# Performance work log

Hardware: AMD Instinct MI355X
Metric: run time of the kernel (lower is better)

The kernel has to match this reference:

```python
import jax, jax.numpy as jnp
import numpy as np

N_ITER = 3


def squash(v):
    # v: [..., out_C]; scale by ||v||^2/(1+||v||^2) and normalize by ||v||
    sq = jnp.sum(v * v, axis=-1, keepdims=True)
    return (sq / (1.0 + sq)) * v / jnp.sqrt(sq)


def setup_inputs() -> dict:
    key = jax.random.key(0)
    k1, k2 = jax.random.split(key)
    B, n_nodes, n_caps, in_C, out_C = 64, 2048, 32, 16, 32
    x = jax.random.normal(k1, (B, n_nodes, in_C), dtype=jnp.float32)
    route_weights = 0.1 * jax.random.normal(k2, (n_nodes, n_caps, in_C, out_C), dtype=jnp.float32)
    return {"x": x, "route_weights": route_weights}


def reference(x, route_weights):
    # priors: [B, n_nodes, n_caps, out_C]
    priors = jnp.einsum('bni,nkio->bnko', x, route_weights)
    logits = jnp.zeros_like(priors)
    outputs = None
    for i in range(N_ITER):
        probs = jax.nn.softmax(logits, axis=2)            # over n_caps
        s = jnp.sum(probs * priors, axis=1, keepdims=True)  # [B,1,n_caps,out_C]
        outputs = squash(s)
        if i != N_ITER - 1:
            delta = jnp.sum(priors * outputs, axis=-1, keepdims=True)
            logits = logits + delta
    return outputs
```

## Files before the change

kernel.cpp:

```cpp
#include <hip/hip_runtime.h>
#include <math.h>


#define BATCH 64
#define NN    2048
#define NK    32
#define NI    16
#define NO    32

#define PNB   16
#define NSETS (NN / PNB)

typedef __bf16 bf16x8 __attribute__((ext_vector_type(8)));
typedef float  f32x16 __attribute__((ext_vector_type(16)));

__device__ __forceinline__ unsigned short f2bf(float f) {
    unsigned int x = __float_as_uint(f);
    unsigned int lsb = (x >> 16) & 1u;
    x += 0x7fffu + lsb;
    return (unsigned short)(x >> 16);
}
__device__ __forceinline__ float bflo(unsigned int u) { return __uint_as_float(u << 16); }
__device__ __forceinline__ float bfhi(unsigned int u) { return __uint_as_float(u & 0xffff0000u); }


__global__ __launch_bounds__(1024) void zero_kernel(float* __restrict__ p) {
    p[blockIdx.x * 1024 + threadIdx.x] = 0.f;
}

__global__ __launch_bounds__(256) void xt_kernel(const float* __restrict__ xg,
                                                 unsigned short* __restrict__ xT) {
    int id = blockIdx.x * 256 + threadIdx.x;
    int b = id >> 13;
    int rem = id & 8191;
    int n = rem >> 2;
    int i4 = rem & 3;
    float4 v = *(const float4*)(xg + ((size_t)b * NN + n) * NI + i4 * 4);
    ushort4 o;
    o.x = f2bf(v.x); o.y = f2bf(v.y); o.z = f2bf(v.z); o.w = f2bf(v.w);
    *(ushort4*)(xT + ((size_t)n * BATCH + b) * NI + i4 * 4) = o;
}

__global__ __launch_bounds__(256) void wqt_kernel(const float* __restrict__ Wg,
                                                  unsigned short* __restrict__ wq) {
    const int w    = threadIdx.x >> 6;
    const int lane = threadIdx.x & 63;
    const int task = blockIdx.x * 4 + w;
    const int o  = lane & 31;
    const int ih = lane >> 5;
    const float* src = Wg + (size_t)task * (NI * NO);
    unsigned short d[8];
#pragma unroll
    for (int j = 0; j < 8; ++j)
        d[j] = f2bf(src[(ih * 8 + j) * NO + o]);
    *(uint4*)(wq + (size_t)task * (NO * NI) + o * NI + ih * 8) = *(uint4*)d;
}

template <int PASS>
__global__ __launch_bounds__(1024) void fused_pass(
    const unsigned short* __restrict__ xT,
    const unsigned short* __restrict__ wq,
    const float* __restrict__ outv,
    float* __restrict__ logits0,
    float* __restrict__ s_glob)
{
    __shared__ float delta_lds[2][32 * 33];

    const int tid  = threadIdx.x;
    const int w    = tid >> 6;
    const int lane = tid & 63;
    const int l5   = lane & 31;
    const int h5   = lane >> 5;
    const int set  = blockIdx.x;
    const int hb   = blockIdx.y;
    const int k0   = 2 * w, k1 = 2 * w + 1;
    const int gb5  = hb * 32 + l5;
    const int sb   = tid >> 5;
    const int sk   = tid & 31;
    const int nbase = set * PNB;

    unsigned orp0[8], orp1[8];
    if constexpr (PASS >= 1) {
#pragma unroll
        for (int q = 0; q < 8; ++q) {
            const int oA = ((2*q) & 3) + 8 * ((2*q) >> 2) + 4 * h5;
            const int oB = ((2*q+1) & 3) + 8 * ((2*q+1) >> 2) + 4 * h5;
            float a0 = outv[(k0 * NO + oA) * BATCH + gb5];
            float b0 = outv[(k0 * NO + oB) * BATCH + gb5];
            float a1 = outv[(k1 * NO + oA) * BATCH + gb5];
            float b1 = outv[(k1 * NO + oB) * BATCH + gb5];
            orp0[q] = (unsigned)f2bf(a0) | ((unsigned)f2bf(b0) << 16);
            orp1[q] = (unsigned)f2bf(a1) | ((unsigned)f2bf(b1) << 16);
        }
    }

    float sa0[16], sa1[16];
#pragma unroll
    for (int r = 0; r < 16; ++r) { sa0[r] = 0.f; sa1[r] = 0.f; }

    bf16x8 aN, b0N, b1N;
    float gN = 0.f;
    {
        const int n = nbase;
        b0N = *(const bf16x8*)(wq + (size_t)n * (NK * NO * NI) + k0 * (NO * NI) + l5 * NI + h5 * 8);
        b1N = *(const bf16x8*)(wq + (size_t)n * (NK * NO * NI) + k1 * (NO * NI) + l5 * NI + h5 * 8);
        aN  = *(const bf16x8*)(xT + (size_t)n * (BATCH * NI) + gb5 * NI + h5 * 8);
        if constexpr (PASS == 2)
            gN = logits0[(size_t)n * (BATCH * NK) + hb * 1024 + tid];
    }

    int buf = 0;
    for (int j = 0; j < PNB; ++j) {
        const int n = nbase + j;
        const bf16x8 aC = aN, b0C = b0N, b1C = b1N;
        const float gC = gN;
        if (j < PNB - 1) {
            const int n2 = n + 1;
            b0N = *(const bf16x8*)(wq + (size_t)n2 * (NK * NO * NI) + k0 * (NO * NI) + l5 * NI + h5 * 8);
            b1N = *(const bf16x8*)(wq + (size_t)n2 * (NK * NO * NI) + k1 * (NO * NI) + l5 * NI + h5 * 8);
            aN  = *(const bf16x8*)(xT + (size_t)n2 * (BATCH * NI) + gb5 * NI + h5 * 8);
            if constexpr (PASS == 2)
                gN = logits0[(size_t)n2 * (BATCH * NK) + hb * 1024 + tid];
        }

        f32x16 c0, c1;
#pragma unroll
        for (int r = 0; r < 16; ++r) { c0[r] = 0.f; c1[r] = 0.f; }
        c0 = __builtin_amdgcn_mfma_f32_32x32x16_bf16(b0C, aC, c0, 0, 0, 0);
        c1 = __builtin_amdgcn_mfma_f32_32x32x16_bf16(b1C, aC, c1, 0, 0, 0);

        if constexpr (PASS == 0) {
#pragma unroll
            for (int r = 0; r < 16; ++r) { sa0[r] += c0[r]; sa1[r] += c1[r]; }
        } else {
            float d0 = 0.f, d1 = 0.f;
#pragma unroll
            for (int r = 0; r < 16; ++r) {
                const unsigned u0 = orp0[r >> 1], u1 = orp1[r >> 1];
                const float o0 = (r & 1) ? bfhi(u0) : bflo(u0);
                const float o1 = (r & 1) ? bfhi(u1) : bflo(u1);
                d0 = fmaf(c0[r], o0, d0);
                d1 = fmaf(c1[r], o1, d1);
            }
            d0 += __shfl_xor(d0, 32);
            d1 += __shfl_xor(d1, 32);

            delta_lds[buf][l5 * 33 + (h5 ? k1 : k0)] = h5 ? d1 : d0;
            __syncthreads();

            float l = delta_lds[buf][sb * 33 + sk];
            if constexpr (PASS == 1)
                logits0[(size_t)n * (BATCH * NK) + hb * 1024 + tid] = l;
            else
                l += gC;
            float e = __expf(l);
            float s = e;
#pragma unroll
            for (int mask = 1; mask < 32; mask <<= 1)
                s += __shfl_xor(s, mask);
            delta_lds[buf][sb * 33 + sk] = e / s;
            __syncthreads();

            const float p0 = delta_lds[buf][l5 * 33 + k0];
            const float p1 = delta_lds[buf][l5 * 33 + k1];
#pragma unroll
            for (int r = 0; r < 16; ++r) {
                sa0[r] = fmaf(p0, c0[r], sa0[r]);
                sa1[r] = fmaf(p1, c1[r], sa1[r]);
            }
            buf ^= 1;
        }
    }

    const float scale = (PASS == 0) ? (1.f / NK) : 1.f;
#pragma unroll
    for (int r = 0; r < 16; ++r) {
        const int o = (r & 3) + 8 * (r >> 2) + 4 * h5;
        atomicAdd(&s_glob[(k0 * NO + o) * BATCH + gb5], sa0[r] * scale);
        atomicAdd(&s_glob[(k1 * NO + o) * BATCH + gb5], sa1[r] * scale);
    }
}

template <int FINAL>
__global__ __launch_bounds__(1024) void reduce_squash2(
    float* __restrict__ s_glob,
    float* __restrict__ outv,
    float* __restrict__ outp)
{
    __shared__ float red[2048];
    __shared__ float coef[64];
    const int k = blockIdx.x;
    const int t = threadIdx.x;
    const int o = t >> 6;
    const int b = t & 63;
    float* base = s_glob + k * 2048;
    float va = base[o * 64 + b];
    float vb = base[(o + 16) * 64 + b];
    base[o * 64 + b] = 0.f;
    base[(o + 16) * 64 + b] = 0.f;
    red[o * 64 + b] = va * va;
    red[(o + 16) * 64 + b] = vb * vb;
    __syncthreads();
    if (t < 64) {
        float sq = 0.f;
#pragma unroll
        for (int oo = 0; oo < 32; ++oo) sq += red[oo * 64 + t];
        coef[t] = sq / ((1.f + sq) * sqrtf(sq));
    }
    __syncthreads();
    const float cf = coef[b];
    if (FINAL) {
        outp[b * 1024 + k * 32 + o]      = va * cf;
        outp[b * 1024 + k * 32 + o + 16] = vb * cf;
    } else {
        outv[k * 2048 + o * 64 + b]        = va * cf;
        outv[k * 2048 + (o + 16) * 64 + b] = vb * cf;
    }
}


#define LBB 32
#define LNCHUNK 8
#define LNBLK (NN / LNCHUNK)
#define LTHREADS 512
#define WK_STRIDE 516

template <int PASS>
__global__ __launch_bounds__(LTHREADS, 1) void legacy_pass(
    const float* __restrict__ xg, const float* __restrict__ Wg,
    const float* __restrict__ outvL, float* __restrict__ logits,
    float* __restrict__ partial)
{
    __shared__ float w_lds[NK * WK_STRIDE];
    __shared__ float x_lds[LBB][NI + 1];
    __shared__ float delta_lds[LBB][NK + 1];
    const int t = threadIdx.x, nb = blockIdx.x, bg = blockIdx.y;
    const int b0 = bg * LBB;
    const int k = t >> 4, bq = t & 15, bl0 = bq * 2, bl1 = bq * 2 + 1;
    float acc0[NO], acc1[NO];
#pragma unroll
    for (int o = 0; o < NO; ++o) { acc0[o] = 0.f; acc1[o] = 0.f; }
    float outr0[NO], outr1[NO];
    if constexpr (PASS >= 1) {
        const float4* o0 = (const float4*)&outvL[((b0 + bl0) * NK + k) * NO];
        const float4* o1 = (const float4*)&outvL[((b0 + bl1) * NK + k) * NO];
#pragma unroll
        for (int q = 0; q < NO / 4; ++q) {
            float4 a = o0[q]; float4 b = o1[q];
            outr0[4*q+0]=a.x; outr0[4*q+1]=a.y; outr0[4*q+2]=a.z; outr0[4*q+3]=a.w;
            outr1[4*q+0]=b.x; outr1[4*q+1]=b.y; outr1[4*q+2]=b.z; outr1[4*q+3]=b.w;
        }
    }
    for (int j = 0; j < LNCHUNK; ++j) {
        const int n = nb * LNCHUNK + j;
        __syncthreads();
        {
            const float4* src = (const float4*)(Wg + (size_t)n * (NK * NI * NO));
#pragma unroll
            for (int r = 0; r < (NK * NI * NO / 4) / LTHREADS; ++r) {
                int idx4 = t + r * LTHREADS;
                float4 v = src[idx4];
                int e = idx4 * 4, kk = e >> 9, rem = e & 511;
                *(float4*)&w_lds[kk * WK_STRIDE + rem] = v;
            }
        }
        { int bl = t >> 4, i = t & 15;
          x_lds[bl][i] = xg[((size_t)(b0 + bl) * NN + n) * NI + i]; }
        __syncthreads();
        if constexpr (PASS == 0) {
#pragma unroll
            for (int i = 0; i < NI; ++i) {
                float xa = x_lds[bl0][i], xb = x_lds[bl1][i];
                const float* wrow = &w_lds[k * WK_STRIDE + i * NO];
#pragma unroll
                for (int o = 0; o < NO; ++o) {
                    float w = wrow[o];
                    acc0[o] = fmaf(xa, w, acc0[o]);
                    acc1[o] = fmaf(xb, w, acc1[o]);
                }
            }
        } else {
            float pr0[NO], pr1[NO];
#pragma unroll
            for (int o = 0; o < NO; ++o) { pr0[o] = 0.f; pr1[o] = 0.f; }
#pragma unroll
            for (int i = 0; i < NI; ++i) {
                float xa = x_lds[bl0][i], xb = x_lds[bl1][i];
                const float* wrow = &w_lds[k * WK_STRIDE + i * NO];
#pragma unroll
                for (int o = 0; o < NO; ++o) {
                    float w = wrow[o];
                    pr0[o] = fmaf(xa, w, pr0[o]);
                    pr1[o] = fmaf(xb, w, pr1[o]);
                }
            }
            float d0 = 0.f, d1 = 0.f;
#pragma unroll
            for (int o = 0; o < NO; ++o) {
                d0 = fmaf(pr0[o], outr0[o], d0);
                d1 = fmaf(pr1[o], outr1[o], d1);
            }
            float l0 = d0, l1 = d1;
            const size_t li0 = ((size_t)(b0 + bl0) * NN + n) * NK + k;
            const size_t li1 = ((size_t)(b0 + bl1) * NN + n) * NK + k;
            if constexpr (PASS == 2) { l0 += logits[li0]; l1 += logits[li1]; }
            else { logits[li0] = d0; logits[li1] = d1; }
            delta_lds[bl0][k] = l0; delta_lds[bl1][k] = l1;
            __syncthreads();
            float m0 = -1e30f, m1 = -1e30f;
#pragma unroll
            for (int kk = 0; kk < NK; ++kk) {
                m0 = fmaxf(m0, delta_lds[bl0][kk]);
                m1 = fmaxf(m1, delta_lds[bl1][kk]);
            }
            float s0 = 0.f, s1 = 0.f;
#pragma unroll
            for (int kk = 0; kk < NK; ++kk) {
                s0 += __expf(delta_lds[bl0][kk] - m0);
                s1 += __expf(delta_lds[bl1][kk] - m1);
            }
            float p0 = __expf(l0 - m0) / s0;
            float p1 = __expf(l1 - m1) / s1;
#pragma unroll
            for (int o = 0; o < NO; ++o) {
                acc0[o] = fmaf(p0, pr0[o], acc0[o]);
                acc1[o] = fmaf(p1, pr1[o], acc1[o]);
            }
        }
    }
    const float scale = (PASS == 0) ? (1.f / NK) : 1.f;
    float4* p0 = (float4*)&partial[(((size_t)nb * BATCH + (b0 + bl0)) * NK + k) * NO];
    float4* p1 = (float4*)&partial[(((size_t)nb * BATCH + (b0 + bl1)) * NK + k) * NO];
#pragma unroll
    for (int q = 0; q < NO / 4; ++q) {
        float4 v0, v1;
        v0.x = acc0[4*q+0]*scale; v0.y = acc0[4*q+1]*scale;
        v0.z = acc0[4*q+2]*scale; v0.w = acc0[4*q+3]*scale;
        v1.x = acc1[4*q+0]*scale; v1.y = acc1[4*q+1]*scale;
        v1.z = acc1[4*q+2]*scale; v1.w = acc1[4*q+3]*scale;
        p0[q] = v0; p1[q] = v1;
    }
}

__global__ __launch_bounds__(256) void legacy_reduce(
    const float* __restrict__ partial, float* __restrict__ outf)
{
    const int tid = blockIdx.x * 256 + threadIdx.x;
    float v = 0.f;
    for (int nb = 0; nb < LNBLK; ++nb)
        v += partial[(size_t)nb * (BATCH * NK * NO) + tid];
    float sq = v * v;
#pragma unroll
    for (int off = 1; off < 32; off <<= 1) sq += __shfl_xor(sq, off);
    float coef = sq / ((1.f + sq) * sqrtf(sq));
    outf[tid] = v * coef;
}


extern "C" void kernel_launch(void* const* d_in, const int* in_sizes, int n_in,
                              void* d_out, int out_size, void* d_ws, size_t ws_size,
                              hipStream_t stream)
{
    const float* xg = (const float*)d_in[0];
    const float* Wg = (const float*)d_in[1];
    float* outp = (float*)d_out;
    char* ws = (char*)d_ws;

    const size_t SZ_WQ     = (size_t)NN * NK * NO * NI * 2;
    const size_t SZ_XT     = (size_t)NN * BATCH * NI * 2;
    const size_t SZ_LOGITS = (size_t)NN * BATCH * NK * 4;
    const size_t SZ_SG     = (size_t)NK * NO * BATCH * 4;
    const size_t SZ_OUTV   = (size_t)NK * NO * BATCH * 4;
    const size_t NEED = SZ_WQ + SZ_XT + SZ_LOGITS + SZ_SG + SZ_OUTV;

    if (ws_size >= NEED) {
        unsigned short* wq = (unsigned short*)ws;
        unsigned short* xT = (unsigned short*)(ws + SZ_WQ);
        float* logits0 = (float*)(ws + SZ_WQ + SZ_XT);
        float* s_glob  = (float*)(ws + SZ_WQ + SZ_XT + SZ_LOGITS);
        float* outv    = (float*)(ws + SZ_WQ + SZ_XT + SZ_LOGITS + SZ_SG);

        zero_kernel<<<64, 1024, 0, stream>>>(s_glob);
        xt_kernel<<<2048, 256, 0, stream>>>(xg, xT);
        wqt_kernel<<<16384, 256, 0, stream>>>(Wg, wq);

        dim3 pg(NSETS, 2);
        fused_pass<0><<<pg, 1024, 0, stream>>>(xT, wq, nullptr, nullptr, s_glob);
        reduce_squash2<0><<<32, 1024, 0, stream>>>(s_glob, outv, nullptr);
        fused_pass<1><<<pg, 1024, 0, stream>>>(xT, wq, outv, logits0, s_glob);
        reduce_squash2<0><<<32, 1024, 0, stream>>>(s_glob, outv, nullptr);
        fused_pass<2><<<pg, 1024, 0, stream>>>(xT, wq, outv, logits0, s_glob);
        reduce_squash2<1><<<32, 1024, 0, stream>>>(s_glob, nullptr, outp);
    } else {
        float* partial = (float*)ws;
        float* logits = (float*)(ws + (size_t)LNBLK * BATCH * NK * NO * 4);
        float* outvL = (float*)(ws + (size_t)LNBLK * BATCH * NK * NO * 4 + (size_t)BATCH * NN * NK * 4);
        dim3 grid(LNBLK, BATCH / LBB);
        const int rblocks = BATCH * NK * NO / 256;
        legacy_pass<0><<<grid, LTHREADS, 0, stream>>>(xg, Wg, nullptr, logits, partial);
        legacy_reduce<<<rblocks, 256, 0, stream>>>(partial, outvL);
        legacy_pass<1><<<grid, LTHREADS, 0, stream>>>(xg, Wg, outvL, logits, partial);
        legacy_reduce<<<rblocks, 256, 0, stream>>>(partial, outvL);
        legacy_pass<2><<<grid, LTHREADS, 0, stream>>>(xg, Wg, outvL, logits, partial);
        legacy_reduce<<<rblocks, 256, 0, stream>>>(partial, outp);
    }
}
```

Measured before the change: 380.0 us.

## Fuse routing passes into one persistent kernel with grid barriers and LDS-resident logits

```diff
diff --git a/kernel.cpp b/kernel.cpp
--- a/kernel.cpp
+++ b/kernel.cpp
@@ -10,9 +10,13 @@
 
 #define PNB   16
 #define NSETS (NN / PNB)
+#define NBLK  (NSETS * 2)
+#define XT_JS 528
 
 typedef __bf16 bf16x8 __attribute__((ext_vector_type(8)));
 typedef float  f32x16 __attribute__((ext_vector_type(16)));
+
+template <int N> struct IC { static constexpr int v = N; };
 
 __device__ __forceinline__ unsigned short f2bf(float f) {
     unsigned int x = __float_as_uint(f);
@@ -23,26 +27,22 @@
 __device__ __forceinline__ float bflo(unsigned int u) { return __uint_as_float(u << 16); }
 __device__ __forceinline__ float bfhi(unsigned int u) { return __uint_as_float(u & 0xffff0000u); }
 
-
-__global__ __launch_bounds__(1024) void zero_kernel(float* __restrict__ p) {
-    p[blockIdx.x * 1024 + threadIdx.x] = 0.f;
-}
-
-__global__ __launch_bounds__(256) void xt_kernel(const float* __restrict__ xg,
-                                                 unsigned short* __restrict__ xT) {
-    int id = blockIdx.x * 256 + threadIdx.x;
-    int b = id >> 13;
-    int rem = id & 8191;
-    int n = rem >> 2;
-    int i4 = rem & 3;
-    float4 v = *(const float4*)(xg + ((size_t)b * NN + n) * NI + i4 * 4);
-    ushort4 o;
-    o.x = f2bf(v.x); o.y = f2bf(v.y); o.z = f2bf(v.z); o.w = f2bf(v.w);
-    *(ushort4*)(xT + ((size_t)n * BATCH + b) * NI + i4 * 4) = o;
-}
-
-__global__ __launch_bounds__(256) void wqt_kernel(const float* __restrict__ Wg,
-                                                  unsigned short* __restrict__ wq) {
+__device__ __forceinline__ void grid_bar(unsigned* __restrict__ bar, int idx) {
+    __syncthreads();
+    if (threadIdx.x == 0) {
+        __builtin_amdgcn_fence(__ATOMIC_RELEASE, "agent");
+        __hip_atomic_fetch_add(&bar[idx], 1u, __ATOMIC_RELAXED, __HIP_MEMORY_SCOPE_AGENT);
+        while (__hip_atomic_load(&bar[idx], __ATOMIC_RELAXED, __HIP_MEMORY_SCOPE_AGENT) < NBLK)
+            __builtin_amdgcn_s_sleep(2);
+        __builtin_amdgcn_fence(__ATOMIC_ACQUIRE, "agent");
+    }
+    __syncthreads();
+}
+
+__global__ __launch_bounds__(256) void prep_kernel(const float* __restrict__ Wg,
+                                                   unsigned short* __restrict__ wq,
+                                                   float* __restrict__ sg3,
+                                                   unsigned* __restrict__ bar) {
     const int w    = threadIdx.x >> 6;
     const int lane = threadIdx.x & 63;
     const int task = blockIdx.x * 4 + w;
@@ -54,16 +54,24 @@
     for (int j = 0; j < 8; ++j)
         d[j] = f2bf(src[(ih * 8 + j) * NO + o]);
     *(uint4*)(wq + (size_t)task * (NO * NI) + o * NI + ih * 8) = *(uint4*)d;
-}
-
-template <int PASS>
-__global__ __launch_bounds__(1024) void fused_pass(
-    const unsigned short* __restrict__ xT,
+
+    if (blockIdx.x < 192) {
+        float4 z = {0.f, 0.f, 0.f, 0.f};
+        *(float4*)(sg3 + (size_t)blockIdx.x * 1024 + threadIdx.x * 4) = z;
+    }
+    if (blockIdx.x == 200 && threadIdx.x < 8) bar[threadIdx.x] = 0u;
+}
+
+
+__global__ __launch_bounds__(1024) void routing_mega(
+    const float* __restrict__ xg,
     const unsigned short* __restrict__ wq,
-    const float* __restrict__ outv,
-    float* __restrict__ logits0,
-    float* __restrict__ s_glob)
+    float* __restrict__ s_glob,
+    unsigned* __restrict__ bar,
+    float* __restrict__ outp)
 {
+    __shared__ unsigned short xt_lds[PNB * XT_JS];
+    __shared__ float logits_lds[PNB * 1024];
     __shared__ float delta_lds[2][32 * 33];
 
     const int tid  = threadIdx.x;
@@ -75,146 +83,162 @@
     const int hb   = blockIdx.y;
     const int k0   = 2 * w, k1 = 2 * w + 1;
     const int gb5  = hb * 32 + l5;
-    const int sb   = tid >> 5;
-    const int sk   = tid & 31;
+    const int sbt  = tid >> 5;
+    const int skt  = tid & 31;
     const int nbase = set * PNB;
 
+#pragma unroll
+    for (int rr = 0; rr < 2; ++rr) {
+        const int id  = tid + rr * 1024;
+        const int bl  = id >> 6;
+        const int rem = id & 63;
+        const int j   = rem >> 2;
+        const int i4  = rem & 3;
+        float4 v = *(const float4*)(xg + ((size_t)(hb * 32 + bl) * NN + (nbase + j)) * NI + i4 * 4);
+        ushort4 o4;
+        o4.x = f2bf(v.x); o4.y = f2bf(v.y); o4.z = f2bf(v.z); o4.w = f2bf(v.w);
+        *(ushort4*)(xt_lds + j * XT_JS + bl * 16 + i4 * 4) = o4;
+    }
+    __syncthreads();
+
     unsigned orp0[8], orp1[8];
-    if constexpr (PASS >= 1) {
+
+    auto build_orp = [&](const float* __restrict__ sbuf) {
+        float v0[16], v1[16];
+        float sq0 = 0.f, sq1 = 0.f;
+#pragma unroll
+        for (int r = 0; r < 16; ++r) {
+            const int o = (r & 3) + 8 * (r >> 2) + 4 * h5;
+            v0[r] = sbuf[(k0 * NO + o) * BATCH + gb5];
+            v1[r] = sbuf[(k1 * NO + o) * BATCH + gb5];
+            sq0 = fmaf(v0[r], v0[r], sq0);
+            sq1 = fmaf(v1[r], v1[r], sq1);
+        }
+        sq0 += __shfl_xor(sq0, 32);
+        sq1 += __shfl_xor(sq1, 32);
+        const float cf0 = sq0 / ((1.f + sq0) * sqrtf(sq0));
+        const float cf1 = sq1 / ((1.f + sq1) * sqrtf(sq1));
 #pragma unroll
         for (int q = 0; q < 8; ++q) {
-            const int oA = ((2*q) & 3) + 8 * ((2*q) >> 2) + 4 * h5;
-            const int oB = ((2*q+1) & 3) + 8 * ((2*q+1) >> 2) + 4 * h5;
-            float a0 = outv[(k0 * NO + oA) * BATCH + gb5];
-            float b0 = outv[(k0 * NO + oB) * BATCH + gb5];
-            float a1 = outv[(k1 * NO + oA) * BATCH + gb5];
-            float b1 = outv[(k1 * NO + oB) * BATCH + gb5];
-            orp0[q] = (unsigned)f2bf(a0) | ((unsigned)f2bf(b0) << 16);
-            orp1[q] = (unsigned)f2bf(a1) | ((unsigned)f2bf(b1) << 16);
-        }
-    }
-
-    float sa0[16], sa1[16];
-#pragma unroll
-    for (int r = 0; r < 16; ++r) { sa0[r] = 0.f; sa1[r] = 0.f; }
-
-    bf16x8 aN, b0N, b1N;
-    float gN = 0.f;
-    {
-        const int n = nbase;
-        b0N = *(const bf16x8*)(wq + (size_t)n * (NK * NO * NI) + k0 * (NO * NI) + l5 * NI + h5 * 8);
-        b1N = *(const bf16x8*)(wq + (size_t)n * (NK * NO * NI) + k1 * (NO * NI) + l5 * NI + h5 * 8);
-        aN  = *(const bf16x8*)(xT + (size_t)n * (BATCH * NI) + gb5 * NI + h5 * 8);
-        if constexpr (PASS == 2)
-            gN = logits0[(size_t)n * (BATCH * NK) + hb * 1024 + tid];
-    }
-
-    int buf = 0;
-    for (int j = 0; j < PNB; ++j) {
-        const int n = nbase + j;
-        const bf16x8 aC = aN, b0C = b0N, b1C = b1N;
-        const float gC = gN;
-        if (j < PNB - 1) {
-            const int n2 = n + 1;
-            b0N = *(const bf16x8*)(wq + (size_t)n2 * (NK * NO * NI) + k0 * (NO * NI) + l5 * NI + h5 * 8);
-            b1N = *(const bf16x8*)(wq + (size_t)n2 * (NK * NO * NI) + k1 * (NO * NI) + l5 * NI + h5 * 8);
-            aN  = *(const bf16x8*)(xT + (size_t)n2 * (BATCH * NI) + gb5 * NI + h5 * 8);
-            if constexpr (PASS == 2)
-                gN = logits0[(size_t)n2 * (BATCH * NK) + hb * 1024 + tid];
-        }
-
-        f32x16 c0, c1;
-#pragma unroll
-        for (int r = 0; r < 16; ++r) { c0[r] = 0.f; c1[r] = 0.f; }
-        c0 = __builtin_amdgcn_mfma_f32_32x32x16_bf16(b0C, aC, c0, 0, 0, 0);
-        c1 = __builtin_amdgcn_mfma_f32_32x32x16_bf16(b1C, aC, c1, 0, 0, 0);
-
-        if constexpr (PASS == 0) {
-#pragma unroll
-            for (int r = 0; r < 16; ++r) { sa0[r] += c0[r]; sa1[r] += c1[r]; }
-        } else {
-            float d0 = 0.f, d1 = 0.f;
-#pragma unroll
-            for (int r = 0; r < 16; ++r) {
-                const unsigned u0 = orp0[r >> 1], u1 = orp1[r >> 1];
-                const float o0 = (r & 1) ? bfhi(u0) : bflo(u0);
-                const float o1 = (r & 1) ? bfhi(u1) : bflo(u1);
-                d0 = fmaf(c0[r], o0, d0);
-                d1 = fmaf(c1[r], o1, d1);
-            }
-            d0 += __shfl_xor(d0, 32);
-            d1 += __shfl_xor(d1, 32);
-
-            delta_lds[buf][l5 * 33 + (h5 ? k1 : k0)] = h5 ? d1 : d0;
-            __syncthreads();
-
-            float l = delta_lds[buf][sb * 33 + sk];
-            if constexpr (PASS == 1)
-                logits0[(size_t)n * (BATCH * NK) + hb * 1024 + tid] = l;
-            else
-                l += gC;
-            float e = __expf(l);
-            float s = e;
-#pragma unroll
-            for (int mask = 1; mask < 32; mask <<= 1)
-                s += __shfl_xor(s, mask);
-            delta_lds[buf][sb * 33 + sk] = e / s;
-            __syncthreads();
-
-            const float p0 = delta_lds[buf][l5 * 33 + k0];
-            const float p1 = delta_lds[buf][l5 * 33 + k1];
-#pragma unroll
-            for (int r = 0; r < 16; ++r) {
-                sa0[r] = fmaf(p0, c0[r], sa0[r]);
-                sa1[r] = fmaf(p1, c1[r], sa1[r]);
-            }
-            buf ^= 1;
-        }
-    }
-
-    const float scale = (PASS == 0) ? (1.f / NK) : 1.f;
-#pragma unroll
-    for (int r = 0; r < 16; ++r) {
-        const int o = (r & 3) + 8 * (r >> 2) + 4 * h5;
-        atomicAdd(&s_glob[(k0 * NO + o) * BATCH + gb5], sa0[r] * scale);
-        atomicAdd(&s_glob[(k1 * NO + o) * BATCH + gb5], sa1[r] * scale);
-    }
-}
-
-template <int FINAL>
-__global__ __launch_bounds__(1024) void reduce_squash2(
-    float* __restrict__ s_glob,
-    float* __restrict__ outv,
-    float* __restrict__ outp)
-{
-    __shared__ float red[2048];
-    __shared__ float coef[64];
-    const int k = blockIdx.x;
-    const int t = threadIdx.x;
-    const int o = t >> 6;
-    const int b = t & 63;
-    float* base = s_glob + k * 2048;
-    float va = base[o * 64 + b];
-    float vb = base[(o + 16) * 64 + b];
-    base[o * 64 + b] = 0.f;
-    base[(o + 16) * 64 + b] = 0.f;
-    red[o * 64 + b] = va * va;
-    red[(o + 16) * 64 + b] = vb * vb;
-    __syncthreads();
-    if (t < 64) {
-        float sq = 0.f;
-#pragma unroll
-        for (int oo = 0; oo < 32; ++oo) sq += red[oo * 64 + t];
-        coef[t] = sq / ((1.f + sq) * sqrtf(sq));
-    }
-    __syncthreads();
-    const float cf = coef[b];
-    if (FINAL) {
+            orp0[q] = (unsigned)f2bf(v0[2 * q] * cf0) | ((unsigned)f2bf(v0[2 * q + 1] * cf0) << 16);
+            orp1[q] = (unsigned)f2bf(v1[2 * q] * cf1) | ((unsigned)f2bf(v1[2 * q + 1] * cf1) << 16);
+        }
+    };
+
+    auto run = [&](auto pcv) {
+        constexpr int PASS = decltype(pcv)::v;
+        float* __restrict__ sg = s_glob + PASS * (NK * NO * BATCH);
+
+        float sa0[16], sa1[16];
+#pragma unroll
+        for (int r = 0; r < 16; ++r) { sa0[r] = 0.f; sa1[r] = 0.f; }
+
+        bf16x8 b0N, b1N;
+        {
+            const int n = nbase;
+            b0N = *(const bf16x8*)(wq + (size_t)n * (NK * NO * NI) + k0 * (NO * NI) + l5 * NI + h5 * 8);
+            b1N = *(const bf16x8*)(wq + (size_t)n * (NK * NO * NI) + k1 * (NO * NI) + l5 * NI + h5 * 8);
+        }
+
+        int buf = 0;
+        for (int j = 0; j < PNB; ++j) {
+            const bf16x8 b0C = b0N, b1C = b1N;
+            if (j < PNB - 1) {
+                const int n2 = nbase + j + 1;
+                b0N = *(const bf16x8*)(wq + (size_t)n2 * (NK * NO * NI) + k0 * (NO * NI) + l5 * NI + h5 * 8);
+                b1N = *(const bf16x8*)(wq + (size_t)n2 * (NK * NO * NI) + k1 * (NO * NI) + l5 * NI + h5 * 8);
+            }
+            const bf16x8 aC = *(const bf16x8*)(xt_lds + j * XT_JS + l5 * 16 + h5 * 8);
+
+            f32x16 c0, c1;
+#pragma unroll
+            for (int r = 0; r < 16; ++r) { c0[r] = 0.f; c1[r] = 0.f; }
+            c0 = __builtin_amdgcn_mfma_f32_32x32x16_bf16(b0C, aC, c0, 0, 0, 0);
+            c1 = __builtin_amdgcn_mfma_f32_32x32x16_bf16(b1C, aC, c1, 0, 0, 0);
+
+            if constexpr (PASS == 0) {
+#pragma unroll
+                for (int r = 0; r < 16; ++r) { sa0[r] += c0[r]; sa1[r] += c1[r]; }
+            } else {
+                float d0 = 0.f, d1 = 0.f;
+#pragma unroll
+                for (int r = 0; r < 16; ++r) {
+                    const unsigned u0 = orp0[r >> 1], u1 = orp1[r >> 1];
+                    const float o0 = (r & 1) ? bfhi(u0) : bflo(u0);
+                    const float o1 = (r & 1) ? bfhi(u1) : bflo(u1);
+                    d0 = fmaf(c0[r], o0, d0);
+                    d1 = fmaf(c1[r], o1, d1);
+                }
+                d0 += __shfl_xor(d0, 32);
+                d1 += __shfl_xor(d1, 32);
+
+                delta_lds[buf][l5 * 33 + (h5 ? k1 : k0)] = h5 ? d1 : d0;
+                __syncthreads();
+
+                float l = delta_lds[buf][sbt * 33 + skt];
+                if constexpr (PASS == 1)
+                    logits_lds[j * 1024 + sbt * 32 + skt] = l;
+                else
+                    l += logits_lds[j * 1024 + sbt * 32 + skt];
+                float e = __expf(l);
+                float s = e;
+#pragma unroll
+                for (int mask = 1; mask < 32; mask <<= 1)
+                    s += __shfl_xor(s, mask);
+                delta_lds[buf][sbt * 33 + skt] = e / s;
+                __syncthreads();
+
+                const float p0 = delta_lds[buf][l5 * 33 + k0];
+                const float p1 = delta_lds[buf][l5 * 33 + k1];
+#pragma unroll
+                for (int r = 0; r < 16; ++r) {
+                    sa0[r] = fmaf(p0, c0[r], sa0[r]);
+                    sa1[r] = fmaf(p1, c1[r], sa1[r]);
+                }
+                buf ^= 1;
+            }
+        }
+
+        const float scale = (PASS == 0) ? (1.f / NK) : 1.f;
+#pragma unroll
+        for (int r = 0; r < 16; ++r) {
+            const int o = (r & 3) + 8 * (r >> 2) + 4 * h5;
+            atomicAdd(&sg[(k0 * NO + o) * BATCH + gb5], sa0[r] * scale);
+            atomicAdd(&sg[(k1 * NO + o) * BATCH + gb5], sa1[r] * scale);
+        }
+    };
+
+    run(IC<0>{});
+    grid_bar(bar, 0);
+    build_orp(s_glob);
+    run(IC<1>{});
+    grid_bar(bar, 1);
+    build_orp(s_glob + NK * NO * BATCH);
+    run(IC<2>{});
+    grid_bar(bar, 2);
+
+    if (hb == 0 && set < NK) {
+        const int k = set;
+        float* red = &delta_lds[0][0];
+        float* cfp = red + 2048;
+        const float* base = s_glob + 2 * (NK * NO * BATCH) + k * (NO * BATCH);
+        const int o = tid >> 6;
+        const int b = tid & 63;
+        const float va = base[o * 64 + b];
+        const float vb = base[(o + 16) * 64 + b];
+        red[o * 64 + b] = va * va;
+        red[(o + 16) * 64 + b] = vb * vb;
+        __syncthreads();
+        if (tid < 64) {
+            float sq = 0.f;
+#pragma unroll
+            for (int oo = 0; oo < 32; ++oo) sq += red[oo * 64 + tid];
+            cfp[tid] = sq / ((1.f + sq) * sqrtf(sq));
+        }
+        __syncthreads();
+        const float cf = cfp[b];
         outp[b * 1024 + k * 32 + o]      = va * cf;
         outp[b * 1024 + k * 32 + o + 16] = vb * cf;
-    } else {
-        outv[k * 2048 + o * 64 + b]        = va * cf;
-        outv[k * 2048 + (o + 16) * 64 + b] = vb * cf;
     }
 }
 
@@ -366,31 +390,18 @@
     float* outp = (float*)d_out;
     char* ws = (char*)d_ws;
 
-    const size_t SZ_WQ     = (size_t)NN * NK * NO * NI * 2;
-    const size_t SZ_XT     = (size_t)NN * BATCH * NI * 2;
-    const size_t SZ_LOGITS = (size_t)NN * BATCH * NK * 4;
-    const size_t SZ_SG     = (size_t)NK * NO * BATCH * 4;
-    const size_t SZ_OUTV   = (size_t)NK * NO * BATCH * 4;
-    const size_t NEED = SZ_WQ + SZ_XT + SZ_LOGITS + SZ_SG + SZ_OUTV;
+    const size_t SZ_WQ  = (size_t)NN * NK * NO * NI * 2;
+    const size_t SZ_SG3 = 3 * (size_t)NK * NO * BATCH * 4;
+    const size_t SZ_BAR = 256;
+    const size_t NEED = SZ_WQ + SZ_SG3 + SZ_BAR;
 
     if (ws_size >= NEED) {
         unsigned short* wq = (unsigned short*)ws;
-        unsigned short* xT = (unsigned short*)(ws + SZ_WQ);
-        float* logits0 = (float*)(ws + SZ_WQ + SZ_XT);
-        float* s_glob  = (float*)(ws + SZ_WQ + SZ_XT + SZ_LOGITS);
-        float* outv    = (float*)(ws + SZ_WQ + SZ_XT + SZ_LOGITS + SZ_SG);
-
-        zero_kernel<<<64, 1024, 0, stream>>>(s_glob);
-        xt_kernel<<<2048, 256, 0, stream>>>(xg, xT);
-        wqt_kernel<<<16384, 256, 0, stream>>>(Wg, wq);
-
-        dim3 pg(NSETS, 2);
-        fused_pass<0><<<pg, 1024, 0, stream>>>(xT, wq, nullptr, nullptr, s_glob);
-        reduce_squash2<0><<<32, 1024, 0, stream>>>(s_glob, outv, nullptr);
-        fused_pass<1><<<pg, 1024, 0, stream>>>(xT, wq, outv, logits0, s_glob);
-        reduce_squash2<0><<<32, 1024, 0, stream>>>(s_glob, outv, nullptr);
-        fused_pass<2><<<pg, 1024, 0, stream>>>(xT, wq, outv, logits0, s_glob);
-        reduce_squash2<1><<<32, 1024, 0, stream>>>(s_glob, nullptr, outp);
+        float* sg3 = (float*)(ws + SZ_WQ);
+        unsigned* bar = (unsigned*)(ws + SZ_WQ + SZ_SG3);
+
+        prep_kernel<<<16384, 256, 0, stream>>>(Wg, wq, sg3, bar);
+        routing_mega<<<dim3(NSETS, 2), 1024, 0, stream>>>(xg, wq, sg3, bar, outp);
     } else {
         float* partial = (float*)ws;
         float* logits = (float*)(ws + (size_t)LNBLK * BATCH * NK * NO * 4);
```

After: 477.8 us. 1.26x slower.

## Fuse x transpose into fused passes and replace atomics with partial-sum reduction

Applied to the files above, without the earlier changes.

```diff
diff --git a/kernel.cpp b/kernel.cpp
--- a/kernel.cpp
+++ b/kernel.cpp
@@ -10,6 +10,7 @@
 
 #define PNB   16
 #define NSETS (NN / PNB)
+#define XT_JS 528
 
 typedef __bf16 bf16x8 __attribute__((ext_vector_type(8)));
 typedef float  f32x16 __attribute__((ext_vector_type(16)));
@@ -22,24 +23,6 @@
 }
 __device__ __forceinline__ float bflo(unsigned int u) { return __uint_as_float(u << 16); }
 __device__ __forceinline__ float bfhi(unsigned int u) { return __uint_as_float(u & 0xffff0000u); }
-
-
-__global__ __launch_bounds__(1024) void zero_kernel(float* __restrict__ p) {
-    p[blockIdx.x * 1024 + threadIdx.x] = 0.f;
-}
-
-__global__ __launch_bounds__(256) void xt_kernel(const float* __restrict__ xg,
-                                                 unsigned short* __restrict__ xT) {
-    int id = blockIdx.x * 256 + threadIdx.x;
-    int b = id >> 13;
-    int rem = id & 8191;
-    int n = rem >> 2;
-    int i4 = rem & 3;
-    float4 v = *(const float4*)(xg + ((size_t)b * NN + n) * NI + i4 * 4);
-    ushort4 o;
-    o.x = f2bf(v.x); o.y = f2bf(v.y); o.z = f2bf(v.z); o.w = f2bf(v.w);
-    *(ushort4*)(xT + ((size_t)n * BATCH + b) * NI + i4 * 4) = o;
-}
 
 __global__ __launch_bounds__(256) void wqt_kernel(const float* __restrict__ Wg,
                                                   unsigned short* __restrict__ wq) {
@@ -58,12 +41,13 @@
 
 template <int PASS>
 __global__ __launch_bounds__(1024) void fused_pass(
-    const unsigned short* __restrict__ xT,
+    const float* __restrict__ xg,
     const unsigned short* __restrict__ wq,
     const float* __restrict__ outv,
     float* __restrict__ logits0,
-    float* __restrict__ s_glob)
+    float* __restrict__ part)
 {
+    __shared__ unsigned short xt_lds[PNB * XT_JS];
     __shared__ float delta_lds[2][32 * 33];
 
     const int tid  = threadIdx.x;
@@ -79,6 +63,20 @@
     const int sk   = tid & 31;
     const int nbase = set * PNB;
 
+#pragma unroll
+    for (int rr = 0; rr < 2; ++rr) {
+        const int id  = tid + rr * 1024;
+        const int bl  = id >> 6;
+        const int rem = id & 63;
+        const int j   = rem >> 2;
+        const int i4  = rem & 3;
+        float4 v = *(const float4*)(xg + ((size_t)(hb * 32 + bl) * NN + (nbase + j)) * NI + i4 * 4);
+        ushort4 o4;
+        o4.x = f2bf(v.x); o4.y = f2bf(v.y); o4.z = f2bf(v.z); o4.w = f2bf(v.w);
+        *(ushort4*)(xt_lds + j * XT_JS + bl * 16 + i4 * 4) = o4;
+    }
+    __syncthreads();
+
     unsigned orp0[8], orp1[8];
     if constexpr (PASS >= 1) {
 #pragma unroll
@@ -98,13 +96,12 @@
 #pragma unroll
     for (int r = 0; r < 16; ++r) { sa0[r] = 0.f; sa1[r] = 0.f; }
 
-    bf16x8 aN, b0N, b1N;
+    bf16x8 b0N, b1N;
     float gN = 0.f;
     {
         const int n = nbase;
         b0N = *(const bf16x8*)(wq + (size_t)n * (NK * NO * NI) + k0 * (NO * NI) + l5 * NI + h5 * 8);
         b1N = *(const bf16x8*)(wq + (size_t)n * (NK * NO * NI) + k1 * (NO * NI) + l5 * NI + h5 * 8);
-        aN  = *(const bf16x8*)(xT + (size_t)n * (BATCH * NI) + gb5 * NI + h5 * 8);
         if constexpr (PASS == 2)
             gN = logits0[(size_t)n * (BATCH * NK) + hb * 1024 + tid];
     }
@@ -112,16 +109,16 @@
     int buf = 0;
     for (int j = 0; j < PNB; ++j) {
         const int n = nbase + j;
-        const bf16x8 aC = aN, b0C = b0N, b1C = b1N;
+        const bf16x8 b0C = b0N, b1C = b1N;
         const float gC = gN;
         if (j < PNB - 1) {
             const int n2 = n + 1;
             b0N = *(const bf16x8*)(wq + (size_t)n2 * (NK * NO * NI) + k0 * (NO * NI) + l5 * NI + h5 * 8);
             b1N = *(const bf16x8*)(wq + (size_t)n2 * (NK * NO * NI) + k1 * (NO * NI) + l5 * NI + h5 * 8);
-            aN  = *(const bf16x8*)(xT + (size_t)n2 * (BATCH * NI) + gb5 * NI + h5 * 8);
             if constexpr (PASS == 2)
                 gN = logits0[(size_t)n2 * (BATCH * NK) + hb * 1024 + tid];
         }
+        const bf16x8 aC = *(const bf16x8*)(xt_lds + j * XT_JS + l5 * 16 + h5 * 8);
 
         f32x16 c0, c1;
 #pragma unroll
@@ -173,48 +170,53 @@
     }
 
     const float scale = (PASS == 0) ? (1.f / NK) : 1.f;
+    float* pb = part + ((size_t)(hb * NSETS + set) << 15);
 #pragma unroll
     for (int r = 0; r < 16; ++r) {
         const int o = (r & 3) + 8 * (r >> 2) + 4 * h5;
-        atomicAdd(&s_glob[(k0 * NO + o) * BATCH + gb5], sa0[r] * scale);
-        atomicAdd(&s_glob[(k1 * NO + o) * BATCH + gb5], sa1[r] * scale);
+        pb[(k0 * NO + o) * 32 + l5] = sa0[r] * scale;
+        pb[(k1 * NO + o) * 32 + l5] = sa1[r] * scale;
     }
 }
 
 template <int FINAL>
-__global__ __launch_bounds__(1024) void reduce_squash2(
-    float* __restrict__ s_glob,
+__global__ __launch_bounds__(1024) void reduce_squash3(
+    const float* __restrict__ part,
     float* __restrict__ outv,
     float* __restrict__ outp)
 {
-    __shared__ float red[2048];
-    __shared__ float coef[64];
-    const int k = blockIdx.x;
-    const int t = threadIdx.x;
-    const int o = t >> 6;
-    const int b = t & 63;
-    float* base = s_glob + k * 2048;
-    float va = base[o * 64 + b];
-    float vb = base[(o + 16) * 64 + b];
-    base[o * 64 + b] = 0.f;
-    base[(o + 16) * 64 + b] = 0.f;
-    red[o * 64 + b] = va * va;
-    red[(o + 16) * 64 + b] = vb * vb;
+    __shared__ float s_lds[32 * 33];
+    __shared__ float cf_lds[32];
+    const int k  = blockIdx.x;
+    const int hb = blockIdx.y;
+    const int t  = threadIdx.x;
+    const int o  = t >> 5;
+    const int b  = t & 31;
+
+    const float* src = part + ((size_t)hb * NSETS << 15) + (k << 10) + (o << 5) + b;
+    float v0 = 0.f, v1 = 0.f, v2 = 0.f, v3 = 0.f;
+#pragma unroll 4
+    for (int s = 0; s < NSETS; s += 4) {
+        v0 += src[(size_t)(s + 0) << 15];
+        v1 += src[(size_t)(s + 1) << 15];
+        v2 += src[(size_t)(s + 2) << 15];
+        v3 += src[(size_t)(s + 3) << 15];
+    }
+    const float v = (v0 + v1) + (v2 + v3);
+    s_lds[o * 33 + b] = v;
     __syncthreads();
-    if (t < 64) {
+    if (t < 32) {
         float sq = 0.f;
 #pragma unroll
-        for (int oo = 0; oo < 32; ++oo) sq += red[oo * 64 + t];
-        coef[t] = sq / ((1.f + sq) * sqrtf(sq));
+        for (int oo = 0; oo < 32; ++oo) { const float x = s_lds[oo * 33 + t]; sq = fmaf(x, x, sq); }
+        cf_lds[t] = sq / ((1.f + sq) * sqrtf(sq));
     }
     __syncthreads();
-    const float cf = coef[b];
     if (FINAL) {
-        outp[b * 1024 + k * 32 + o]      = va * cf;
-        outp[b * 1024 + k * 32 + o + 16] = vb * cf;
+        const int bq = t >> 5, oq = t & 31;
+        outp[(size_t)(hb * 32 + bq) * 1024 + k * 32 + oq] = s_lds[oq * 33 + bq] * cf_lds[bq];
     } else {
-        outv[k * 2048 + o * 64 + b]        = va * cf;
-        outv[k * 2048 + (o + 16) * 64 + b] = vb * cf;
+        outv[k * 2048 + o * 64 + hb * 32 + b] = v * cf_lds[b];
     }
 }
 
@@ -367,30 +369,27 @@
     char* ws = (char*)d_ws;
 
     const size_t SZ_WQ     = (size_t)NN * NK * NO * NI * 2;
-    const size_t SZ_XT     = (size_t)NN * BATCH * NI * 2;
+    const size_t SZ_PART   = (size_t)256 * 32768 * 4;
     const size_t SZ_LOGITS = (size_t)NN * BATCH * NK * 4;
-    const size_t SZ_SG     = (size_t)NK * NO * BATCH * 4;
     const size_t SZ_OUTV   = (size_t)NK * NO * BATCH * 4;
-    const size_t NEED = SZ_WQ + SZ_XT + SZ_LOGITS + SZ_SG + SZ_OUTV;
+    const size_t NEED = SZ_WQ + SZ_PART + SZ_LOGITS + SZ_OUTV;
 
     if (ws_size >= NEED) {
         unsigned short* wq = (unsigned short*)ws;
-        unsigned short* xT = (unsigned short*)(ws + SZ_WQ);
-        float* logits0 = (float*)(ws + SZ_WQ + SZ_XT);
-        float* s_glob  = (float*)(ws + SZ_WQ + SZ_XT + SZ_LOGITS);
-        float* outv    = (float*)(ws + SZ_WQ + SZ_XT + SZ_LOGITS + SZ_SG);
-
-        zero_kernel<<<64, 1024, 0, stream>>>(s_glob);
-        xt_kernel<<<2048, 256, 0, stream>>>(xg, xT);
+        float* part    = (float*)(ws + SZ_WQ);
+        float* logits0 = (float*)(ws + SZ_WQ + SZ_PART);
+        float* outv    = (float*)(ws + SZ_WQ + SZ_PART + SZ_LOGITS);
+
         wqt_kernel<<<16384, 256, 0, stream>>>(Wg, wq);
 
         dim3 pg(NSETS, 2);
-        fused_pass<0><<<pg, 1024, 0, stream>>>(xT, wq, nullptr, nullptr, s_glob);
-        reduce_squash2<0><<<32, 1024, 0, stream>>>(s_glob, outv, nullptr);
-        fused_pass<1><<<pg, 1024, 0, stream>>>(xT, wq, outv, logits0, s_glob);
-        reduce_squash2<0><<<32, 1024, 0, stream>>>(s_glob, outv, nullptr);
-        fused_pass<2><<<pg, 1024, 0, stream>>>(xT, wq, outv, logits0, s_glob);
-        reduce_squash2<1><<<32, 1024, 0, stream>>>(s_glob, nullptr, outp);
+        dim3 rg(NK, 2);
+        fused_pass<0><<<pg, 1024, 0, stream>>>(xg, wq, nullptr, nullptr, part);
+        reduce_squash3<0><<<rg, 1024, 0, stream>>>(part, outv, nullptr);
+        fused_pass<1><<<pg, 1024, 0, stream>>>(xg, wq, outv, logits0, part);
+        reduce_squash3<0><<<rg, 1024, 0, stream>>>(part, outv, nullptr);
+        fused_pass<2><<<pg, 1024, 0, stream>>>(xg, wq, outv, logits0, part);
+        reduce_squash3<1><<<rg, 1024, 0, stream>>>(part, nullptr, outp);
     } else {
         float* partial = (float*)ws;
         float* logits = (float*)(ws + (size_t)LNBLK * BATCH * NK * NO * 4);
```

Result: faster. 334.0 us (-12.1%).
